# Optimization experiments

Hardware: AMD Instinct MI355X
Metric: run time of the kernel (lower is better)

Reference implementation:

```python
import jax, jax.numpy as jnp
import numpy as np

# Model dims (match init_kwargs): dim=768, num_heads=12, num_kv_heads=2 -> G=6, head_dim=64
DIM, HKV, G, D = 768, 2, 6, 64


def setup_inputs() -> dict:
    key = jax.random.key(0)
    ks = jax.random.split(key, 9)
    w = 0.02  # init scale for weights
    return {
        "x": jax.random.normal(ks[0], (8, 1024, DIM), dtype=jnp.float32),
        "depth_k": jax.random.normal(ks[1], (8, 1024, HKV, D), dtype=jnp.float32),
        "depth_v": jax.random.normal(ks[2], (8, 1024, HKV, D), dtype=jnp.float32),
        "Wq": jax.random.normal(ks[3], (DIM, DIM), dtype=jnp.float32) * w,
        "bq": jnp.zeros((DIM,), dtype=jnp.float32),
        "Wkv": jax.random.normal(ks[4], (2 * HKV * D, DIM), dtype=jnp.float32) * w,
        "bkv": jnp.zeros((2 * HKV * D,), dtype=jnp.float32),
        "Wproj": jax.random.normal(ks[5], (DIM, DIM), dtype=jnp.float32) * w,
        "bproj": jnp.zeros((DIM,), dtype=jnp.float32),
    }


def reference(x, depth_k, depth_v, Wq, bq, Wkv, bkv, Wproj, bproj):
    B, N, C = x.shape
    scale = D ** -0.5
    # Q projection, GQA groups unfolded into the sequence dim: [B, N*G, Hkv, D]
    q = (x @ Wq.T + bq).reshape(B, N * G, HKV, D)
    # KV projection: [B, N, 2, Hkv, D]
    kv = (x @ Wkv.T + bkv).reshape(B, N, 2, HKV, D)
    k, v = kv[:, :, 0], kv[:, :, 1]
    # Concatenate depth (previous-layer) KV cache along the sequence dim
    k_full = jnp.concatenate([depth_k, k], axis=1)  # [B, N_cache+N, Hkv, D]
    v_full = jnp.concatenate([depth_v, v], axis=1)
    # Full (non-causal) attention per kv head over the unfolded query sequence
    scores = jnp.einsum('bqhd,bkhd->bhqk', q, k_full) * scale  # [B, Hkv, N*G, Kv]
    attn = jax.nn.softmax(scores, axis=-1)
    o = jnp.einsum('bhqk,bkhd->bqhd', attn, v_full)  # [B, N*G, Hkv, D]
    out = o.reshape(B, N, C) @ Wproj.T + bproj  # fold G*Hkv*D back to C=dim
    return out, k, v
```

## Files before the change

### kernel.cpp

```cpp
#include <hip/hip_runtime.h>

using sh8 = __attribute__((ext_vector_type(8))) short;
using sh4 = __attribute__((ext_vector_type(4))) short;
using fx4 = __attribute__((ext_vector_type(4))) float;

#define MFMA(a,b,c)   __builtin_amdgcn_mfma_f32_16x16x32_bf16((a),(b),(c),0,0,0)
#define MFMA16(a,b,c) __builtin_amdgcn_mfma_f32_16x16x16bf16_1k((a),(b),(c),0,0,0)

__device__ __forceinline__ short f2bf(float f) {
    union { float f; unsigned u; } v; v.f = f;
    return (short)((v.u + 0x7fffu + ((v.u >> 16) & 1u)) >> 16);
}

__device__ __forceinline__ unsigned bfpair(float lo, float hi) {
    unsigned ul = __float_as_uint(lo) + 0x8000u;
    unsigned uh = __float_as_uint(hi) + 0x8000u;
    return __builtin_amdgcn_perm(uh, ul, 0x07060302);
}

__device__ __forceinline__ sh8 pack8(float4 a, float4 b) {
    union { unsigned u[4]; sh8 s; } r;
    r.u[0] = bfpair(a.x, a.y);
    r.u[1] = bfpair(a.z, a.w);
    r.u[2] = bfpair(b.x, b.y);
    r.u[3] = bfpair(b.z, b.w);
    return r.s;
}

__device__ __forceinline__ sh4 lo4(sh8 v) { return __builtin_shufflevector(v, v, 0, 1, 2, 3); }
__device__ __forceinline__ sh4 hi4(sh8 v) { return __builtin_shufflevector(v, v, 4, 5, 6, 7); }

#define QSCALE 0.18033688011112042f

__global__ __launch_bounds__(256) void prep_k(const float* __restrict__ x,
                                              const float* __restrict__ Wq,
                                              const float* __restrict__ bq,
                                              const float* __restrict__ Wkv,
                                              const float* __restrict__ bkv,
                                              const float* __restrict__ dk,
                                              const float* __restrict__ dv,
                                              float* __restrict__ ok,
                                              float* __restrict__ ov,
                                              short* __restrict__ q_ws,
                                              short* __restrict__ k_ws,
                                              short* __restrict__ vT_ws)
{
    __shared__ alignas(16) short Al[128 * 40];
    __shared__ alignas(16) short Bl[128 * 40];
    const int blk = blockIdx.x;
    const int t   = threadIdx.x;

    if (blk < 512) {
        const bool isq = (blk < 384);
        const int  i   = isq ? blk : blk - 384;
        const int  nbx = isq ? 6 : 2;
        const int  bm  = (i / nbx) * 128, bn = (i % nbx) * 128;
        const float* Wmat = isq ? Wq : Wkv;

        const int wave = t >> 6, lane = t & 63;
        const int wm   = wave >> 1, wn = wave & 1;
        const int lhi  = lane >> 4, llo = lane & 15;

        const int srow = t >> 1, scol = (t & 1) * 16;
        const float* ap = x    + (size_t)(bm + srow) * 768 + scol;
        const float* bp = Wmat + (size_t)(bn + srow) * 768 + scol;

        fx4 zero = {0.f, 0.f, 0.f, 0.f};
        fx4 acc[4][4];
        #pragma unroll
        for (int a = 0; a < 4; ++a)
            #pragma unroll
            for (int b2 = 0; b2 < 4; ++b2) acc[a][b2] = zero;

        float4 pa0 = *(const float4*)(ap);     float4 pa1 = *(const float4*)(ap + 4);
        float4 pa2 = *(const float4*)(ap + 8); float4 pa3 = *(const float4*)(ap + 12);
        float4 pb0 = *(const float4*)(bp);     float4 pb1 = *(const float4*)(bp + 4);
        float4 pb2 = *(const float4*)(bp + 8); float4 pb3 = *(const float4*)(bp + 12);

        for (int k0 = 0; k0 < 768; k0 += 32) {
            __syncthreads();
            *(sh8*)&Al[srow*40 + scol]     = pack8(pa0, pa1);
            *(sh8*)&Al[srow*40 + scol + 8] = pack8(pa2, pa3);
            *(sh8*)&Bl[srow*40 + scol]     = pack8(pb0, pb1);
            *(sh8*)&Bl[srow*40 + scol + 8] = pack8(pb2, pb3);
            __syncthreads();
            if (k0 + 32 < 768) {
                pa0 = *(const float4*)(ap + k0+32);  pa1 = *(const float4*)(ap + k0+36);
                pa2 = *(const float4*)(ap + k0+40);  pa3 = *(const float4*)(ap + k0+44);
                pb0 = *(const float4*)(bp + k0+32);  pb1 = *(const float4*)(bp + k0+36);
                pb2 = *(const float4*)(bp + k0+40);  pb3 = *(const float4*)(bp + k0+44);
            }
            sh8 af[4], bf[4];
            #pragma unroll
            for (int mt = 0; mt < 4; ++mt)
                af[mt] = *(const sh8*)&Al[(wm*64 + mt*16 + llo)*40 + lhi*8];
            #pragma unroll
            for (int nt = 0; nt < 4; ++nt)
                bf[nt] = *(const sh8*)&Bl[(wn*64 + nt*16 + llo)*40 + lhi*8];
            #pragma unroll
            for (int mt = 0; mt < 4; ++mt)
                #pragma unroll
                for (int nt = 0; nt < 4; ++nt)
                    acc[mt][nt] = MFMA(af[mt], bf[nt], acc[mt][nt]);
        }

        if (isq) {
            #pragma unroll
            for (int nt = 0; nt < 4; ++nt) {
                const int c = bn + wn*64 + nt*16 + llo;
                const float bias = bq[c];
                const int g = c >> 7, h = (c >> 6) & 1, d = c & 63;
                #pragma unroll
                for (int mt = 0; mt < 4; ++mt) {
                    const int m0 = bm + wm*64 + mt*16 + lhi*4;
                    #pragma unroll
                    for (int r = 0; r < 4; ++r) {
                        const int m = m0 + r;
                        const int b = m >> 10, n = m & 1023;
                        const float val = (acc[mt][nt][r] + bias) * QSCALE;
                        q_ws[((size_t)(b*2 + h)*6144 + n*6 + g)*64 + d] = f2bf(val);
                    }
                }
            }
        } else {
            #pragma unroll
            for (int nt = 0; nt < 4; ++nt) {
                const int c = bn + wn*64 + nt*16 + llo;
                const float bias = bkv[c];
                const int s = c >> 7, h = (c >> 6) & 1, d = c & 63;
                #pragma unroll
                for (int mt = 0; mt < 4; ++mt) {
                    const int m0 = bm + wm*64 + mt*16 + lhi*4;
                    const int b = m0 >> 10, n0 = m0 & 1023;
                    float vals[4];
                    #pragma unroll
                    for (int r = 0; r < 4; ++r) vals[r] = acc[mt][nt][r] + bias;
                    if (s == 0) {
                        #pragma unroll
                        for (int r = 0; r < 4; ++r) {
                            ok[((size_t)(b*1024 + n0 + r)*2 + h)*64 + d] = vals[r];
                            k_ws[((size_t)(b*2 + h)*2048 + 1024 + n0 + r)*64 + d] = f2bf(vals[r]);
                        }
                    } else {
                        #pragma unroll
                        for (int r = 0; r < 4; ++r)
                            ov[((size_t)(b*1024 + n0 + r)*2 + h)*64 + d] = vals[r];
                        short4 pk = make_short4(f2bf(vals[0]), f2bf(vals[1]),
                                                f2bf(vals[2]), f2bf(vals[3]));
                        *(short4*)&vT_ws[((size_t)((b*2 + h)*64 + d))*2048 + 1024 + n0] = pk;
                    }
                }
            }
        }
    } else if (blk < 1536) {
        const size_t idx4 = ((size_t)(blk - 512) * 256 + t) * 4;
        const int b  = (int)(idx4 >> 17);
        const int rm = (int)(idx4 & 131071);
        const int tt = rm >> 7, h = (rm >> 6) & 1, d = rm & 63;
        float4 v = *(const float4*)(dk + idx4);
        short4 pk = make_short4(f2bf(v.x), f2bf(v.y), f2bf(v.z), f2bf(v.w));
        *(short4*)&k_ws[((size_t)(b*2 + h)*2048 + tt)*64 + d] = pk;
    } else {
        short (*tl)[72] = (short (*)[72])Al;
        const int tile = blk - 1536;
        const int bh = tile >> 4, tb = tile & 15;
        const int b = bh >> 1, h = bh & 1, t0 = tb * 64;
        const int tt = t >> 2, d0 = (t & 3) * 16;
        const float* src = dv + ((size_t)(b*1024 + t0 + tt)*2 + h)*64 + d0;
        float4 v0 = *(const float4*)(src);
        float4 v1 = *(const float4*)(src + 4);
        float4 v2 = *(const float4*)(src + 8);
        float4 v3 = *(const float4*)(src + 12);
        *(sh8*)&tl[tt][d0]     = pack8(v0, v1);
        *(sh8*)&tl[tt][d0 + 8] = pack8(v2, v3);
        __syncthreads();
        const int d = t >> 2, ts0 = (t & 3) * 16;
        sh8 o0, o1;
        #pragma unroll
        for (int i = 0; i < 8; ++i) o0[i] = tl[ts0 + i][d];
        #pragma unroll
        for (int i = 0; i < 8; ++i) o1[i] = tl[ts0 + 8 + i][d];
        short* dst = vT_ws + ((size_t)((b*2 + h)*64 + d))*2048 + t0 + ts0;
        *(sh8*)dst       = o0;
        *(sh8*)(dst + 8) = o1;
    }
}

__global__ __launch_bounds__(256) void attn_k(const short* __restrict__ q_ws,
                                              const short* __restrict__ k_ws,
                                              const short* __restrict__ vT_ws,
                                              short* __restrict__ o_ws)
{
    __shared__ alignas(16) short Kl[2][64][72];
    __shared__ alignas(16) short Vt[2][64][72];
    const int t    = threadIdx.x;
    const int wave = t >> 6, lane = t & 63;
    const int lhi  = lane >> 4, llo = lane & 15;
    const int bh   = blockIdx.y;
    const int b    = bh >> 1, h = bh & 1;
    const int qt   = blockIdx.x;

    const short* qb = q_ws + ((size_t)bh*6144 + qt*192 + wave*48) * 64;
    sh8 qf[3][2];
    #pragma unroll
    for (int s = 0; s < 3; ++s) {
        qf[s][0] = *(const sh8*)(qb + (s*16 + llo)*64 + lhi*8);
        qf[s][1] = *(const sh8*)(qb + (s*16 + llo)*64 + lhi*8 + 32);
    }

    const short* kbase = k_ws  + (size_t)bh * 2048 * 64;
    const short* vbase = vT_ws + (size_t)bh * 64 * 2048;

    const int urow = t >> 3, uc = t & 7;
    const int vc1  = ((uc & 1) * 2) * 16 + (uc >> 1) * 4;

    const short* kp = kbase + t * 8;
    const short* vp = vbase + (size_t)urow * 2048 + uc * 8;

    {
        sh8 k0 = *(const sh8*)(kp);
        sh8 k1 = *(const sh8*)(kp + 2048);
        sh8 v0 = *(const sh8*)(vp);
        sh8 v1 = *(const sh8*)(vp + 65536);
        *(sh8*)&Kl[0][urow][uc*8]          = k0;
        *(sh8*)&Kl[0][urow + 32][uc*8]     = k1;
        *(sh4*)&Vt[0][urow][vc1]           = lo4(v0);
        *(sh4*)&Vt[0][urow][vc1 + 16]      = hi4(v0);
        *(sh4*)&Vt[0][urow + 32][vc1]      = lo4(v1);
        *(sh4*)&Vt[0][urow + 32][vc1 + 16] = hi4(v1);
    }
    __syncthreads();

    fx4 zero = {0.f, 0.f, 0.f, 0.f};
    fx4 oacc[3][4];
    #pragma unroll
    for (int s = 0; s < 3; ++s)
        #pragma unroll
        for (int dt = 0; dt < 4; ++dt) oacc[s][dt] = zero;
    float lsum[3] = {0.f, 0.f, 0.f};

    for (int kb = 0; kb < 32; ++kb) {
        const int cur = kb & 1, nxt = cur ^ 1;

        sh8 kn0, kn1, vn0, vn1;
        if (kb < 31) {
            kn0 = *(const sh8*)(kp + (kb+1)*4096);
            kn1 = *(const sh8*)(kp + (kb+1)*4096 + 2048);
            vn0 = *(const sh8*)(vp + (kb+1)*64);
            vn1 = *(const sh8*)(vp + (kb+1)*64 + 65536);
        }

        sh4 vts[4][4];
        #pragma unroll
        for (int dt = 0; dt < 4; ++dt) {
            sh8 va = *(const sh8*)&Vt[cur][dt*16 + llo][lhi*16];
            sh8 vb = *(const sh8*)&Vt[cur][dt*16 + llo][lhi*16 + 8];
            vts[0][dt] = lo4(va); vts[1][dt] = hi4(va);
            vts[2][dt] = lo4(vb); vts[3][dt] = hi4(vb);
        }

        #pragma unroll
        for (int nt = 0; nt < 4; ++nt) {
            sh8 kf0 = *(const sh8*)&Kl[cur][nt*16 + llo][lhi*8];
            sh8 kf1 = *(const sh8*)&Kl[cur][nt*16 + llo][lhi*8 + 32];
            #pragma unroll
            for (int s = 0; s < 3; ++s) {
                fx4 st = MFMA(kf0, qf[s][0], zero);
                st     = MFMA(kf1, qf[s][1], st);
                float p0 = __builtin_amdgcn_exp2f(st[0]);
                float p1 = __builtin_amdgcn_exp2f(st[1]);
                float p2 = __builtin_amdgcn_exp2f(st[2]);
                float p3 = __builtin_amdgcn_exp2f(st[3]);
                lsum[s] += (p0 + p1) + (p2 + p3);
                union { unsigned u[2]; sh4 s4; } pu;
                pu.u[0] = bfpair(p0, p1);
                pu.u[1] = bfpair(p2, p3);
                #pragma unroll
                for (int dt = 0; dt < 4; ++dt)
                    oacc[s][dt] = MFMA16(pu.s4, vts[nt][dt], oacc[s][dt]);
            }
        }

        if (kb < 31) {
            *(sh8*)&Kl[nxt][urow][uc*8]          = kn0;
            *(sh8*)&Kl[nxt][urow + 32][uc*8]     = kn1;
            *(sh4*)&Vt[nxt][urow][vc1]           = lo4(vn0);
            *(sh4*)&Vt[nxt][urow][vc1 + 16]      = hi4(vn0);
            *(sh4*)&Vt[nxt][urow + 32][vc1]      = lo4(vn1);
            *(sh4*)&Vt[nxt][urow + 32][vc1 + 16] = hi4(vn1);
        }
        __syncthreads();
    }

    float inv[3];
    #pragma unroll
    for (int s = 0; s < 3; ++s) {
        float v = lsum[s];
        v += __shfl_xor(v, 16, 64);
        v += __shfl_xor(v, 32, 64);
        inv[s] = 1.0f / v;
    }

    #pragma unroll
    for (int s = 0; s < 3; ++s) {
        #pragma unroll
        for (int r = 0; r < 4; ++r) {
            const float iq = __shfl(inv[s], lhi*4 + r, 64);
            const int qi = qt*192 + wave*48 + s*16 + lhi*4 + r;
            const int n = qi / 6, g = qi % 6;
            short* orow = o_ws + ((size_t)(b*1024 + n))*768 + g*128 + h*64;
            #pragma unroll
            for (int dt = 0; dt < 4; ++dt)
                orow[dt*16 + llo] = f2bf(oacc[s][dt][r] * iq);
        }
    }
}

__global__ __launch_bounds__(256) void projgemm_k(const short* __restrict__ o_ws,
                                                  const float* __restrict__ Wp,
                                                  const float* __restrict__ bpj,
                                                  float* __restrict__ out)
{
    __shared__ alignas(16) short Al[128 * 40];
    __shared__ alignas(16) short Bl[128 * 40];
    const int t    = threadIdx.x;
    const int wave = t >> 6, lane = t & 63;
    const int wm   = wave >> 1, wn = wave & 1;
    const int lhi  = lane >> 4, llo = lane & 15;
    const int bm   = blockIdx.y * 128, bn = blockIdx.x * 128;

    const int srow = t >> 1, scol = (t & 1) * 16;
    const short* ap = o_ws + (size_t)(bm + srow) * 768 + scol;
    const float* bp = Wp   + (size_t)(bn + srow) * 768 + scol;

    fx4 zero = {0.f, 0.f, 0.f, 0.f};
    fx4 acc[4][4];
    #pragma unroll
    for (int i = 0; i < 4; ++i)
        #pragma unroll
        for (int j = 0; j < 4; ++j) acc[i][j] = zero;

    sh8 qa0 = *(const sh8*)(ap), qa1 = *(const sh8*)(ap + 8);
    float4 pb0 = *(const float4*)(bp);     float4 pb1 = *(const float4*)(bp + 4);
    float4 pb2 = *(const float4*)(bp + 8); float4 pb3 = *(const float4*)(bp + 12);

    for (int k0 = 0; k0 < 768; k0 += 32) {
        __syncthreads();
        *(sh8*)&Al[srow*40 + scol]     = qa0;
        *(sh8*)&Al[srow*40 + scol + 8] = qa1;
        *(sh8*)&Bl[srow*40 + scol]     = pack8(pb0, pb1);
        *(sh8*)&Bl[srow*40 + scol + 8] = pack8(pb2, pb3);
        __syncthreads();
        if (k0 + 32 < 768) {
            qa0 = *(const sh8*)(ap + k0+32);  qa1 = *(const sh8*)(ap + k0+40);
            pb0 = *(const float4*)(bp + k0+32);  pb1 = *(const float4*)(bp + k0+36);
            pb2 = *(const float4*)(bp + k0+40);  pb3 = *(const float4*)(bp + k0+44);
        }
        sh8 af[4], bf[4];
        #pragma unroll
        for (int mt = 0; mt < 4; ++mt)
            af[mt] = *(const sh8*)&Al[(wm*64 + mt*16 + llo)*40 + lhi*8];
        #pragma unroll
        for (int nt = 0; nt < 4; ++nt)
            bf[nt] = *(const sh8*)&Bl[(wn*64 + nt*16 + llo)*40 + lhi*8];
        #pragma unroll
        for (int mt = 0; mt < 4; ++mt)
            #pragma unroll
            for (int nt = 0; nt < 4; ++nt)
                acc[mt][nt] = MFMA(af[mt], bf[nt], acc[mt][nt]);
    }

    #pragma unroll
    for (int nt = 0; nt < 4; ++nt) {
        const int c = bn + wn*64 + nt*16 + llo;
        const float bias = bpj[c];
        #pragma unroll
        for (int mt = 0; mt < 4; ++mt) {
            const int m0 = bm + wm*64 + mt*16 + lhi*4;
            #pragma unroll
            for (int r = 0; r < 4; ++r)
                out[(size_t)(m0 + r)*768 + c] = acc[mt][nt][r] + bias;
        }
    }
}

extern "C" void kernel_launch(void* const* d_in, const int* in_sizes, int n_in,
                              void* d_out, int out_size, void* d_ws, size_t ws_size,
                              hipStream_t stream)
{
    const float* x   = (const float*)d_in[0];
    const float* dk  = (const float*)d_in[1];
    const float* dv  = (const float*)d_in[2];
    const float* Wq  = (const float*)d_in[3];
    const float* bq  = (const float*)d_in[4];
    const float* Wkv = (const float*)d_in[5];
    const float* bkv = (const float*)d_in[6];
    const float* Wp  = (const float*)d_in[7];
    const float* bpj = (const float*)d_in[8];

    float* out = (float*)d_out;
    float* ok  = out + 6291456;
    float* ov  = out + 7340032;

    char* ws = (char*)d_ws;
    short* q_ws  = (short*)(ws);
    short* k_ws  = (short*)(ws + 12582912);
    short* vT_ws = (short*)(ws + 16777216);
    short* o_ws  = (short*)(ws + 20971520);

    prep_k     <<<dim3(1792),   256, 0, stream>>>(x, Wq, bq, Wkv, bkv, dk, dv,
                                                  ok, ov, q_ws, k_ws, vT_ws);
    attn_k     <<<dim3(32, 16), 256, 0, stream>>>(q_ws, k_ws, vT_ws, o_ws);
    projgemm_k <<<dim3(6, 64),  256, 0, stream>>>(o_ws, Wp, bpj, out);
}
```

Baseline: 224.8 us.

## Pre-swizzle K/V into MFMA fragment order and drop LDS staging in attention

The prep kernel now writes K and transposed V into a layout that matches MFMA register fragments, so each attention lane loads its operands straight from global memory with contiguous 16-byte loads. Shared memory and the barriers around it are gone; loads are double-buffered in registers. The PV product moves to the 16x16x32 MFMA, and the softmax row sum is computed by an MFMA against a ones vector instead of shuffles. The risk is that every workgroup now reads K/V from global or L2 with no LDS reuse across waves, and the V transpose in prep becomes scattered strided reads.

```diff
diff --git a/kernel.cpp b/kernel.cpp
--- a/kernel.cpp
+++ b/kernel.cpp
@@ -5,7 +5,6 @@
 using fx4 = __attribute__((ext_vector_type(4))) float;
 
 #define MFMA(a,b,c)   __builtin_amdgcn_mfma_f32_16x16x32_bf16((a),(b),(c),0,0,0)
-#define MFMA16(a,b,c) __builtin_amdgcn_mfma_f32_16x16x16bf16_1k((a),(b),(c),0,0,0)
 
 __device__ __forceinline__ short f2bf(float f) {
     union { float f; unsigned u; } v; v.f = f;
@@ -27,10 +26,8 @@
     return r.s;
 }
 
-__device__ __forceinline__ sh4 lo4(sh8 v) { return __builtin_shufflevector(v, v, 0, 1, 2, 3); }
-__device__ __forceinline__ sh4 hi4(sh8 v) { return __builtin_shufflevector(v, v, 4, 5, 6, 7); }
-
 #define QSCALE 0.18033688011112042f
+
 
 __global__ __launch_bounds__(256) void prep_k(const float* __restrict__ x,
                                               const float* __restrict__ Wq,
@@ -135,19 +132,30 @@
                     float vals[4];
                     #pragma unroll
                     for (int r = 0; r < 4; ++r) vals[r] = acc[mt][nt][r] + bias;
+                    const int key = 1024 + n0;
                     if (s == 0) {
                         #pragma unroll
-                        for (int r = 0; r < 4; ++r) {
+                        for (int r = 0; r < 4; ++r)
                             ok[((size_t)(b*1024 + n0 + r)*2 + h)*64 + d] = vals[r];
-                            k_ws[((size_t)(b*2 + h)*2048 + 1024 + n0 + r)*64 + d] = f2bf(vals[r]);
-                        }
+                        const int kb_ = key >> 6, nt_ = (key >> 4) & 3;
+                        const int half = d >> 5, lhiK = (d >> 3) & 3, j = d & 7;
+                        const size_t base = (size_t)(b*2 + h)*131072
+                            + (size_t)(((((kb_*4 + nt_)*2 + half)*64) + lhiK*16 + (key & 15))*8 + j);
+                        #pragma unroll
+                        for (int r = 0; r < 4; ++r)
+                            k_ws[base + r*8] = f2bf(vals[r]);
                     } else {
                         #pragma unroll
                         for (int r = 0; r < 4; ++r)
                             ov[((size_t)(b*1024 + n0 + r)*2 + h)*64 + d] = vals[r];
+                        const int kb_ = key >> 6, g_ = (key >> 5) & 1, k5 = key & 31;
+                        const int half5 = k5 >> 4, lhi5 = (k5 >> 2) & 3;
+                        const int dt_ = d >> 4, llov = d & 15;
                         short4 pk = make_short4(f2bf(vals[0]), f2bf(vals[1]),
                                                 f2bf(vals[2]), f2bf(vals[3]));
-                        *(short4*)&vT_ws[((size_t)((b*2 + h)*64 + d))*2048 + 1024 + n0] = pk;
+                        const size_t base = (size_t)(b*2 + h)*131072
+                            + (size_t)(((((kb_*2 + g_)*4 + dt_)*64) + lhi5*16 + llov)*8 + half5*4);
+                        *(short4*)&vT_ws[base] = pk;
                     }
                 }
             }
@@ -159,30 +167,25 @@
         const int tt = rm >> 7, h = (rm >> 6) & 1, d = rm & 63;
         float4 v = *(const float4*)(dk + idx4);
         short4 pk = make_short4(f2bf(v.x), f2bf(v.y), f2bf(v.z), f2bf(v.w));
-        *(short4*)&k_ws[((size_t)(b*2 + h)*2048 + tt)*64 + d] = pk;
+        const int kb_ = tt >> 6, nt_ = (tt >> 4) & 3, lloK = tt & 15;
+        const int half = d >> 5, lhiK = (d >> 3) & 3, j = d & 7;
+        const size_t addr = (size_t)(b*2 + h)*131072
+            + (size_t)(((((kb_*4 + nt_)*2 + half)*64) + lhiK*16 + lloK)*8 + j);
+        *(short4*)&k_ws[addr] = pk;
     } else {
-        short (*tl)[72] = (short (*)[72])Al;
-        const int tile = blk - 1536;
-        const int bh = tile >> 4, tb = tile & 15;
-        const int b = bh >> 1, h = bh & 1, t0 = tb * 64;
-        const int tt = t >> 2, d0 = (t & 3) * 16;
-        const float* src = dv + ((size_t)(b*1024 + t0 + tt)*2 + h)*64 + d0;
-        float4 v0 = *(const float4*)(src);
-        float4 v1 = *(const float4*)(src + 4);
-        float4 v2 = *(const float4*)(src + 8);
-        float4 v3 = *(const float4*)(src + 12);
-        *(sh8*)&tl[tt][d0]     = pack8(v0, v1);
-        *(sh8*)&tl[tt][d0 + 8] = pack8(v2, v3);
-        __syncthreads();
-        const int d = t >> 2, ts0 = (t & 3) * 16;
-        sh8 o0, o1;
-        #pragma unroll
-        for (int i = 0; i < 8; ++i) o0[i] = tl[ts0 + i][d];
-        #pragma unroll
-        for (int i = 0; i < 8; ++i) o1[i] = tl[ts0 + 8 + i][d];
-        short* dst = vT_ws + ((size_t)((b*2 + h)*64 + d))*2048 + t0 + ts0;
-        *(sh8*)dst       = o0;
-        *(sh8*)(dst + 8) = o1;
+        const int unit = (blk - 1536)*4 + (t >> 6);
+        const int lane = t & 63, lhi = lane >> 4, llo = lane & 15;
+        const int dt_ = unit & 3, g_ = (unit >> 2) & 1;
+        const int kb_ = (unit >> 3) & 15, bh = unit >> 7;
+        const int b = bh >> 1, h = bh & 1;
+        const float* s0 = dv
+            + ((size_t)((b*1024 + kb_*64 + g_*32 + lhi*4)*2 + h))*64 + dt_*16 + llo;
+        union { short s[8]; sh8 v8; } o;
+        #pragma unroll
+        for (int jj = 0; jj < 4; ++jj) o.s[jj]     = f2bf(s0[(size_t)jj * 128]);
+        #pragma unroll
+        for (int jj = 0; jj < 4; ++jj) o.s[4 + jj] = f2bf(s0[(size_t)(16 + jj) * 128]);
+        *(sh8*)&vT_ws[((size_t)bh*256 + (kb_*2 + g_)*4 + dt_)*512 + lane*8] = o.v8;
     }
 }
 
@@ -191,8 +194,6 @@
                                               const short* __restrict__ vT_ws,
                                               short* __restrict__ o_ws)
 {
-    __shared__ alignas(16) short Kl[2][64][72];
-    __shared__ alignas(16) short Vt[2][64][72];
     const int t    = threadIdx.x;
     const int wave = t >> 6, lane = t & 63;
     const int lhi  = lane >> 4, llo = lane & 15;
@@ -208,104 +209,76 @@
         qf[s][1] = *(const sh8*)(qb + (s*16 + llo)*64 + lhi*8 + 32);
     }
 
-    const short* kbase = k_ws  + (size_t)bh * 2048 * 64;
-    const short* vbase = vT_ws + (size_t)bh * 64 * 2048;
-
-    const int urow = t >> 3, uc = t & 7;
-    const int vc1  = ((uc & 1) * 2) * 16 + (uc >> 1) * 4;
-
-    const short* kp = kbase + t * 8;
-    const short* vp = vbase + (size_t)urow * 2048 + uc * 8;
-
-    {
-        sh8 k0 = *(const sh8*)(kp);
-        sh8 k1 = *(const sh8*)(kp + 2048);
-        sh8 v0 = *(const sh8*)(vp);
-        sh8 v1 = *(const sh8*)(vp + 65536);
-        *(sh8*)&Kl[0][urow][uc*8]          = k0;
-        *(sh8*)&Kl[0][urow + 32][uc*8]     = k1;
-        *(sh4*)&Vt[0][urow][vc1]           = lo4(v0);
-        *(sh4*)&Vt[0][urow][vc1 + 16]      = hi4(v0);
-        *(sh4*)&Vt[0][urow + 32][vc1]      = lo4(v1);
-        *(sh4*)&Vt[0][urow + 32][vc1 + 16] = hi4(v1);
-    }
-    __syncthreads();
+    const short* kp = k_ws  + (size_t)bh*131072 + lane*8;
+    const short* vp = vT_ws + (size_t)bh*131072 + lane*8;
 
     fx4 zero = {0.f, 0.f, 0.f, 0.f};
     fx4 oacc[3][4];
-    #pragma unroll
-    for (int s = 0; s < 3; ++s)
+    fx4 lacc[3];
+    #pragma unroll
+    for (int s = 0; s < 3; ++s) {
+        lacc[s] = zero;
         #pragma unroll
         for (int dt = 0; dt < 4; ++dt) oacc[s][dt] = zero;
-    float lsum[3] = {0.f, 0.f, 0.f};
-
-    for (int kb = 0; kb < 32; ++kb) {
-        const int cur = kb & 1, nxt = cur ^ 1;
-
-        sh8 kn0, kn1, vn0, vn1;
-        if (kb < 31) {
-            kn0 = *(const sh8*)(kp + (kb+1)*4096);
-            kn1 = *(const sh8*)(kp + (kb+1)*4096 + 2048);
-            vn0 = *(const sh8*)(vp + (kb+1)*64);
-            vn1 = *(const sh8*)(vp + (kb+1)*64 + 65536);
-        }
-
-        sh4 vts[4][4];
-        #pragma unroll
-        for (int dt = 0; dt < 4; ++dt) {
-            sh8 va = *(const sh8*)&Vt[cur][dt*16 + llo][lhi*16];
-            sh8 vb = *(const sh8*)&Vt[cur][dt*16 + llo][lhi*16 + 8];
-            vts[0][dt] = lo4(va); vts[1][dt] = hi4(va);
-            vts[2][dt] = lo4(vb); vts[3][dt] = hi4(vb);
-        }
-
-        #pragma unroll
-        for (int nt = 0; nt < 4; ++nt) {
-            sh8 kf0 = *(const sh8*)&Kl[cur][nt*16 + llo][lhi*8];
-            sh8 kf1 = *(const sh8*)&Kl[cur][nt*16 + llo][lhi*8 + 32];
-            #pragma unroll
-            for (int s = 0; s < 3; ++s) {
-                fx4 st = MFMA(kf0, qf[s][0], zero);
-                st     = MFMA(kf1, qf[s][1], st);
-                float p0 = __builtin_amdgcn_exp2f(st[0]);
-                float p1 = __builtin_amdgcn_exp2f(st[1]);
-                float p2 = __builtin_amdgcn_exp2f(st[2]);
-                float p3 = __builtin_amdgcn_exp2f(st[3]);
-                lsum[s] += (p0 + p1) + (p2 + p3);
-                union { unsigned u[2]; sh4 s4; } pu;
-                pu.u[0] = bfpair(p0, p1);
-                pu.u[1] = bfpair(p2, p3);
-                #pragma unroll
-                for (int dt = 0; dt < 4; ++dt)
-                    oacc[s][dt] = MFMA16(pu.s4, vts[nt][dt], oacc[s][dt]);
-            }
-        }
-
-        if (kb < 31) {
-            *(sh8*)&Kl[nxt][urow][uc*8]          = kn0;
-            *(sh8*)&Kl[nxt][urow + 32][uc*8]     = kn1;
-            *(sh4*)&Vt[nxt][urow][vc1]           = lo4(vn0);
-            *(sh4*)&Vt[nxt][urow][vc1 + 16]      = hi4(vn0);
-            *(sh4*)&Vt[nxt][urow + 32][vc1]      = lo4(vn1);
-            *(sh4*)&Vt[nxt][urow + 32][vc1 + 16] = hi4(vn1);
-        }
-        __syncthreads();
-    }
-
-    float inv[3];
+    }
+
+    union { unsigned u[4]; sh8 s8; } onesu;
+    onesu.u[0] = onesu.u[1] = onesu.u[2] = onesu.u[3] = 0x3F803F80u;
+    const sh8 ones = onesu.s8;
+
+    auto loadg = [&](sh8& K0, sh8& K1, sh8& K2, sh8& K3,
+                     sh8& V0, sh8& V1, sh8& V2, sh8& V3, int it) {
+        const short* kq = kp + (size_t)it * 2048;
+        const short* vq = vp + (size_t)it * 2048;
+        K0 = *(const sh8*)(kq);        K1 = *(const sh8*)(kq + 512);
+        K2 = *(const sh8*)(kq + 1024); K3 = *(const sh8*)(kq + 1536);
+        V0 = *(const sh8*)(vq);        V1 = *(const sh8*)(vq + 512);
+        V2 = *(const sh8*)(vq + 1024); V3 = *(const sh8*)(vq + 1536);
+    };
+
+    auto compg = [&](sh8 K0, sh8 K1, sh8 K2, sh8 K3,
+                     sh8 V0, sh8 V1, sh8 V2, sh8 V3) {
+        #pragma unroll
+        for (int s = 0; s < 3; ++s) {
+            fx4 stA = MFMA(K0, qf[s][0], zero); stA = MFMA(K1, qf[s][1], stA);
+            fx4 stB = MFMA(K2, qf[s][0], zero); stB = MFMA(K3, qf[s][1], stB);
+            float pa0 = __builtin_amdgcn_exp2f(stA[0]);
+            float pa1 = __builtin_amdgcn_exp2f(stA[1]);
+            float pa2 = __builtin_amdgcn_exp2f(stA[2]);
+            float pa3 = __builtin_amdgcn_exp2f(stA[3]);
+            float pb0 = __builtin_amdgcn_exp2f(stB[0]);
+            float pb1 = __builtin_amdgcn_exp2f(stB[1]);
+            float pb2 = __builtin_amdgcn_exp2f(stB[2]);
+            float pb3 = __builtin_amdgcn_exp2f(stB[3]);
+            union { unsigned u[4]; sh8 s8; } pu;
+            pu.u[0] = bfpair(pa0, pa1);
+            pu.u[1] = bfpair(pa2, pa3);
+            pu.u[2] = bfpair(pb0, pb1);
+            pu.u[3] = bfpair(pb2, pb3);
+            lacc[s]    = MFMA(pu.s8, ones, lacc[s]);
+            oacc[s][0] = MFMA(pu.s8, V0, oacc[s][0]);
+            oacc[s][1] = MFMA(pu.s8, V1, oacc[s][1]);
+            oacc[s][2] = MFMA(pu.s8, V2, oacc[s][2]);
+            oacc[s][3] = MFMA(pu.s8, V3, oacc[s][3]);
+        }
+    };
+
+    sh8 xk0, xk1, xk2, xk3, xv0, xv1, xv2, xv3;
+    sh8 yk0, yk1, yk2, yk3, yv0, yv1, yv2, yv3;
+
+    loadg(xk0, xk1, xk2, xk3, xv0, xv1, xv2, xv3, 0);
+    for (int it = 0; it < 64; it += 2) {
+        loadg(yk0, yk1, yk2, yk3, yv0, yv1, yv2, yv3, it + 1);
+        compg(xk0, xk1, xk2, xk3, xv0, xv1, xv2, xv3);
+        loadg(xk0, xk1, xk2, xk3, xv0, xv1, xv2, xv3, (it + 2 < 64) ? it + 2 : 63);
+        compg(yk0, yk1, yk2, yk3, yv0, yv1, yv2, yv3);
+    }
+
     #pragma unroll
     for (int s = 0; s < 3; ++s) {
-        float v = lsum[s];
-        v += __shfl_xor(v, 16, 64);
-        v += __shfl_xor(v, 32, 64);
-        inv[s] = 1.0f / v;
-    }
-
-    #pragma unroll
-    for (int s = 0; s < 3; ++s) {
         #pragma unroll
         for (int r = 0; r < 4; ++r) {
-            const float iq = __shfl(inv[s], lhi*4 + r, 64);
+            const float iq = 1.0f / lacc[s][r];
             const int qi = qt*192 + wave*48 + s*16 + lhi*4 + r;
             const int n = qi / 6, g = qi % 6;
             short* orow = o_ws + ((size_t)(b*1024 + n))*768 + g*128 + h*64;
@@ -408,7 +381,7 @@
     short* vT_ws = (short*)(ws + 16777216);
     short* o_ws  = (short*)(ws + 20971520);
 
-    prep_k     <<<dim3(1792),   256, 0, stream>>>(x, Wq, bq, Wkv, bkv, dk, dv,
+    prep_k     <<<dim3(2048),   256, 0, stream>>>(x, Wq, bq, Wkv, bkv, dk, dv,
                                                   ok, ov, q_ws, k_ws, vT_ws);
     attn_k     <<<dim3(32, 16), 256, 0, stream>>>(q_ws, k_ws, vT_ws, o_ws);
     projgemm_k <<<dim3(6, 64),  256, 0, stream>>>(o_ws, Wp, bpj, out);
```

Result: faster. 213.3 us (-5.1%).
